# Kernel optimization log

Measured on AMD Instinct MI355X. Metric: run time of the kernel, lower is better.

## Reference

```python
import jax, jax.numpy as jnp
import numpy as np

N = 50000
D = 64
E = 800000


def setup_inputs() -> dict:
    key = jax.random.key(0)
    ks = jax.random.split(key, 8)
    x = jax.random.normal(ks[0], (N, D), dtype=jnp.float32)
    edge_index = jax.random.randint(ks[1], (2, E), 0, N, dtype=jnp.int64)
    edge_attr = jax.random.normal(ks[2], (E,), dtype=jnp.float32)
    x_agg_emb = jax.random.normal(ks[3], (N, D), dtype=jnp.float32)
    # Linear(2D -> D) weights stored as [in, out]; scale ~ kaiming-ish
    W_msg = jax.random.normal(ks[4], (2 * D, D), dtype=jnp.float32) * (1.0 / np.sqrt(2 * D))
    b_msg = jnp.zeros((D,), dtype=jnp.float32)
    W_upd = jax.random.normal(ks[5], (2 * D, D), dtype=jnp.float32) * (1.0 / np.sqrt(2 * D))
    b_upd = jnp.zeros((D,), dtype=jnp.float32)
    return {"x": x, "edge_index": edge_index, "edge_attr": edge_attr,
            "x_agg_emb": x_agg_emb, "W_msg": W_msg, "b_msg": b_msg,
            "W_upd": W_upd, "b_upd": b_upd}


def reference(x, edge_index, edge_attr, x_agg_emb, W_msg, b_msg, W_upd, b_upd):
    col, row = edge_index[0], edge_index[1]
    # edge-weighted gather: [E, D]
    msgs = edge_attr[:, None] * x[col]
    # scatter-mean over destination nodes (dim_size = N)
    summed = jax.ops.segment_sum(msgs, row, num_segments=N)            # [N, D]
    counts = jax.ops.segment_sum(jnp.ones_like(edge_attr), row, num_segments=N)  # [N]
    x_agg = summed / jnp.maximum(counts, 1.0)[:, None]
    # message MLP: Linear(2D->D) + ReLU
    m = jax.nn.relu(jnp.concatenate([x_agg, x_agg_emb], axis=-1) @ W_msg + b_msg)
    # update MLP: Linear(2D->D) + ReLU
    out = jax.nn.relu(jnp.concatenate([x, m], axis=-1) @ W_upd + b_upd)
    return out
```

## Files before the change

kernel.cpp:

```cpp
#include <hip/hip_runtime.h>


#define CAP 48
#define FILLB 2048

typedef __attribute__((ext_vector_type(8))) short short8;
typedef __attribute__((ext_vector_type(4))) float f32x4;

__device__ __forceinline__ unsigned short f2bf(float f) {
    unsigned int u = __float_as_uint(f);
    u += 0x7FFFu + ((u >> 16) & 1u);
    return (unsigned short)(u >> 16);
}
__device__ __forceinline__ uint4 pack8(const float* v) {
    uint4 r;
    r.x = (unsigned)f2bf(v[0]) | ((unsigned)f2bf(v[1]) << 16);
    r.y = (unsigned)f2bf(v[2]) | ((unsigned)f2bf(v[3]) << 16);
    r.z = (unsigned)f2bf(v[4]) | ((unsigned)f2bf(v[5]) << 16);
    r.w = (unsigned)f2bf(v[6]) | ((unsigned)f2bf(v[7]) << 16);
    return r;
}

__global__ __launch_bounds__(256) void zero_f32(float* p, int n) {
    int i = blockIdx.x * 256 + threadIdx.x;
    if (i < n) p[i] = 0.0f;
}
__global__ __launch_bounds__(256) void zero_i32(int* p, int n) {
    int i = blockIdx.x * 256 + threadIdx.x;
    if (i < n) p[i] = 0;
}

__global__ __launch_bounds__(256) void fill_group_kernel(
    const int* __restrict__ ei, const float* __restrict__ ea,
    int* cnt, int2* __restrict__ packed, int E, int N)
{
    const int g   = blockIdx.x & 7;
    const int bg  = blockIdx.x >> 3;
    const int nb  = gridDim.x >> 3;
    const int rpg = (N + 7) >> 3;
    const int rlo = g * rpg;
    const int rhi = min(rlo + rpg, N);
    const int chunk = (E + nb - 1) / nb;
    const int lo = bg * chunk;
    const int hi = min(lo + chunk, E);
    int e = lo + (int)threadIdx.x;
    for (; e + 768 < hi; e += 1024) {
        int r0 = ei[E + e];
        int r1 = ei[E + e + 256];
        int r2 = ei[E + e + 512];
        int r3 = ei[E + e + 768];
        int c0 = ei[e], c1 = ei[e + 256], c2 = ei[e + 512], c3 = ei[e + 768];
        float a0 = ea[e], a1 = ea[e + 256], a2 = ea[e + 512], a3 = ea[e + 768];
        bool m0 = (r0 >= rlo) & (r0 < rhi);
        bool m1 = (r1 >= rlo) & (r1 < rhi);
        bool m2 = (r2 >= rlo) & (r2 < rhi);
        bool m3 = (r3 >= rlo) & (r3 < rhi);
        int p0 = CAP, p1 = CAP, p2 = CAP, p3 = CAP;
        if (m0) p0 = atomicAdd(&cnt[r0], 1);
        if (m1) p1 = atomicAdd(&cnt[r1], 1);
        if (m2) p2 = atomicAdd(&cnt[r2], 1);
        if (m3) p3 = atomicAdd(&cnt[r3], 1);
        if (m0 && p0 < CAP) packed[(size_t)r0 * CAP + p0] = make_int2(c0, __float_as_int(a0));
        if (m1 && p1 < CAP) packed[(size_t)r1 * CAP + p1] = make_int2(c1, __float_as_int(a1));
        if (m2 && p2 < CAP) packed[(size_t)r2 * CAP + p2] = make_int2(c2, __float_as_int(a2));
        if (m3 && p3 < CAP) packed[(size_t)r3 * CAP + p3] = make_int2(c3, __float_as_int(a3));
    }
    for (; e < hi; e += 256) {
        int row = ei[E + e];
        if (row >= rlo && row < rhi) {
            int pos = atomicAdd(&cnt[row], 1);
            if (pos < CAP)
                packed[(size_t)row * CAP + pos] = make_int2(ei[e], __float_as_int(ea[e]));
        }
    }
}


__device__ __forceinline__ void stage_W1024(
    unsigned short* Wb, const float* Wg, int t)
{
    int R = t >> 6, nn = t & 63;
    int kt = R >> 2, qq = R & 3;
    const float* src = Wg + (size_t)(kt * 32 + qq * 8) * 64 + nn;
    float v[8];
    #pragma unroll
    for (int j = 0; j < 8; j++) v[j] = src[(size_t)j * 64];
    *(uint4*)&Wb[R * 528 + nn * 8] = pack8(v);
}

__global__ __launch_bounds__(1024) void gather_mlp(
    const int2* __restrict__ packed, const int* __restrict__ cnt,
    const float* __restrict__ x, const float* __restrict__ emb,
    const float* __restrict__ Wm, const float* __restrict__ bm,
    const float* __restrict__ Wu, const float* __restrict__ bu,
    float* __restrict__ out, int N)
{
    __shared__ __align__(16) unsigned short Ab[64 * 128];
    __shared__ __align__(16) unsigned short Wb[16 * 528];

    const int t    = threadIdx.x;
    const int g    = blockIdx.x & 7;
    const int tile = blockIdx.x >> 3;
    const int rpg  = (N + 7) >> 3;
    const int rlo  = g * rpg;
    const int rhi  = min(rlo + rpg, N);
    const int tile0 = rlo + tile * 64;
    const int w    = t >> 6;
    const int lane = t & 63;
    const int q = lane >> 4, ln = lane & 15;

    stage_W1024(Wb, Wm, t);
    if (t < 512) {
        int r = t >> 3, c = t & 7;
        int node = tile0 + r;
        float v[8] = {0.f, 0.f, 0.f, 0.f, 0.f, 0.f, 0.f, 0.f};
        if (node < rhi) {
            const float* src = emb + (size_t)node * 64 + c * 8;
            float4 p0 = ((const float4*)src)[0];
            float4 p1 = ((const float4*)src)[1];
            v[0] = p0.x; v[1] = p0.y; v[2] = p0.z; v[3] = p0.w;
            v[4] = p1.x; v[5] = p1.y; v[6] = p1.z; v[7] = p1.w;
        }
        int ch = 8 + c;
        *(uint4*)&Ab[r * 128 + ((ch ^ (r & 15)) * 8)] = pack8(v);
    }

    for (int i = 0; i < 4; i++) {
        int r = w * 4 + i;
        int node = tile0 + r;
        float mean = 0.f;
        if (node < rhi) {
            const int2* seg = packed + (size_t)node * CAP;
            int deg = cnt[node];
            int dl = min(deg, CAP);
            float a0 = 0.f, a1 = 0.f, a2 = 0.f, a3 = 0.f;
            int j = 0;
            for (; j + 4 <= dl; j += 4) {
                int4 q0 = ((const int4*)seg)[(j >> 1)];
                int4 q1 = ((const int4*)seg)[(j >> 1) + 1];
                a0 += __int_as_float(q0.y) * x[(size_t)q0.x * 64 + lane];
                a1 += __int_as_float(q0.w) * x[(size_t)q0.z * 64 + lane];
                a2 += __int_as_float(q1.y) * x[(size_t)q1.x * 64 + lane];
                a3 += __int_as_float(q1.w) * x[(size_t)q1.z * 64 + lane];
            }
            for (; j < dl; j++) {
                int2 p = seg[j];
                a0 += __int_as_float(p.y) * x[(size_t)p.x * 64 + lane];
            }
            mean = ((a0 + a1) + (a2 + a3)) / fmaxf((float)deg, 1.0f);
        }
        int ch = lane >> 3;
        Ab[r * 128 + ((ch ^ (r & 15)) * 8) + (lane & 7)] = f2bf(mean);
    }
    __syncthreads();

    const int wr = w & 3, wn = w >> 2;
    f32x4 acc = (f32x4){0.f, 0.f, 0.f, 0.f};
    {
        const int rr = wr * 16 + ln;
        #pragma unroll
        for (int kt = 0; kt < 4; kt++) {
            short8 af = *(const short8*)&Ab[rr * 128 + (((kt * 4 + q) ^ ln) * 8)];
            short8 bf = *(const short8*)&Wb[(kt * 4 + q) * 528 + (wn * 16 + ln) * 8];
            acc = __builtin_amdgcn_mfma_f32_16x16x32_bf16(af, bf, acc, 0, 0, 0);
        }
    }
    __syncthreads();

    stage_W1024(Wb, Wu, t);
    if (t < 512) {
        int r = t >> 3, c = t & 7;
        int node = tile0 + r;
        float v[8] = {0.f, 0.f, 0.f, 0.f, 0.f, 0.f, 0.f, 0.f};
        if (node < rhi) {
            const float* src = x + (size_t)node * 64 + c * 8;
            float4 p0 = ((const float4*)src)[0];
            float4 p1 = ((const float4*)src)[1];
            v[0] = p0.x; v[1] = p0.y; v[2] = p0.z; v[3] = p0.w;
            v[4] = p1.x; v[5] = p1.y; v[6] = p1.z; v[7] = p1.w;
        }
        *(uint4*)&Ab[r * 128 + ((c ^ (r & 15)) * 8)] = pack8(v);
    }
    {
        float bmv = bm[wn * 16 + ln];
        #pragma unroll
        for (int reg = 0; reg < 4; reg++) {
            float mv = fmaxf(acc[reg] + bmv, 0.f);
            int rr = wr * 16 + q * 4 + reg;
            int k  = 64 + wn * 16 + ln;
            int ch = k >> 3;
            Ab[rr * 128 + ((ch ^ (rr & 15)) * 8) + (k & 7)] = f2bf(mv);
        }
    }
    __syncthreads();

    f32x4 acc2 = (f32x4){0.f, 0.f, 0.f, 0.f};
    {
        const int rr = wr * 16 + ln;
        #pragma unroll
        for (int kt = 0; kt < 4; kt++) {
            short8 af = *(const short8*)&Ab[rr * 128 + (((kt * 4 + q) ^ ln) * 8)];
            short8 bf = *(const short8*)&Wb[(kt * 4 + q) * 528 + (wn * 16 + ln) * 8];
            acc2 = __builtin_amdgcn_mfma_f32_16x16x32_bf16(af, bf, acc2, 0, 0, 0);
        }
    }
    {
        float buv = bu[wn * 16 + ln];
        #pragma unroll
        for (int reg = 0; reg < 4; reg++) {
            int rr = wr * 16 + q * 4 + reg;
            int node = tile0 + rr;
            if (node < rhi)
                out[(size_t)node * 64 + wn * 16 + ln] =
                    fmaxf(acc2[reg] + buv, 0.f);
        }
    }
}


__global__ __launch_bounds__(256) void hist_kernel(
    const int* __restrict__ ei, int* hist, int E)
{
    int e = blockIdx.x * 256 + threadIdx.x;
    if (e < E) atomicAdd(&hist[ei[E + e]], 1);
}
__global__ __launch_bounds__(256) void scan_partial_kernel(
    const int* __restrict__ hist, int* partial, int N)
{
    __shared__ int s[256];
    int t = threadIdx.x;
    int i = blockIdx.x * 256 + t;
    s[t] = (i < N) ? hist[i] : 0;
    __syncthreads();
    #pragma unroll
    for (int off = 128; off > 0; off >>= 1) {
        if (t < off) s[t] += s[t + off];
        __syncthreads();
    }
    if (t == 0) partial[blockIdx.x] = s[0];
}
__global__ __launch_bounds__(256) void scan_top_kernel(
    const int* __restrict__ partial, int* scanP, int NB)
{
    __shared__ int s[256];
    int t = threadIdx.x;
    int v = (t < NB) ? partial[t] : 0;
    s[t] = v;
    __syncthreads();
    #pragma unroll
    for (int off = 1; off < 256; off <<= 1) {
        int add = (t >= off) ? s[t - off] : 0;
        __syncthreads();
        s[t] += add;
        __syncthreads();
    }
    if (t < NB) scanP[t] = s[t] - v;
}
__global__ __launch_bounds__(256) void scan_final_kernel(
    const int* __restrict__ hist, const int* __restrict__ scanP,
    int* offsets, int* cursor, int N)
{
    __shared__ int s[256];
    int t = threadIdx.x;
    int i = blockIdx.x * 256 + t;
    int v = (i < N) ? hist[i] : 0;
    s[t] = v;
    __syncthreads();
    #pragma unroll
    for (int off = 1; off < 256; off <<= 1) {
        int add = (t >= off) ? s[t - off] : 0;
        __syncthreads();
        s[t] += add;
        __syncthreads();
    }
    if (i < N) {
        int o = scanP[blockIdx.x] + s[t] - v;
        offsets[i] = o;
        cursor[i]  = o;
    }
}
__global__ __launch_bounds__(256) void fill_kernel(
    const int* __restrict__ ei, const float* __restrict__ ea,
    int* cursor, int2* __restrict__ packed, int E)
{
    int e = blockIdx.x * 256 + threadIdx.x;
    if (e >= E) return;
    int pos = atomicAdd(&cursor[ei[E + e]], 1);
    packed[pos] = make_int2(ei[e], __float_as_int(ea[e]));
}
__global__ __launch_bounds__(256) void gather_kernel(
    const int2* __restrict__ packed, const int* __restrict__ offsets,
    const int* __restrict__ hist, const float* __restrict__ x,
    float* __restrict__ out, int N)
{
    int t = threadIdx.x;
    int n = blockIdx.x * 4 + (t >> 6);
    int lane = t & 63;
    if (n >= N) return;
    int start = offsets[n];
    int deg   = hist[n];
    float a0 = 0.f, a1 = 0.f, a2 = 0.f, a3 = 0.f;
    int j = 0;
    for (; j + 4 <= deg; j += 4) {
        int2 p0 = packed[start + j];
        int2 p1 = packed[start + j + 1];
        int2 p2 = packed[start + j + 2];
        int2 p3 = packed[start + j + 3];
        a0 += __int_as_float(p0.y) * x[(size_t)p0.x * 64 + lane];
        a1 += __int_as_float(p1.y) * x[(size_t)p1.x * 64 + lane];
        a2 += __int_as_float(p2.y) * x[(size_t)p2.x * 64 + lane];
        a3 += __int_as_float(p3.y) * x[(size_t)p3.x * 64 + lane];
    }
    for (; j < deg; j++) {
        int2 p = packed[start + j];
        a0 += __int_as_float(p.y) * x[(size_t)p.x * 64 + lane];
    }
    float acc = (a0 + a1) + (a2 + a3);
    out[(size_t)n * 64 + lane] = acc / fmaxf((float)deg, 1.0f);
}


__global__ __launch_bounds__(256) void scatter_kernel(
    const int* __restrict__ ei, const float* __restrict__ ea,
    const float* __restrict__ x, float* summed, float* counts, int E)
{
    int idx = blockIdx.x * 256 + threadIdx.x;
    int e = idx >> 6;
    int d = idx & 63;
    if (e >= E) return;
    float v = ea[e] * x[(size_t)ei[e] * 64 + d];
    atomicAdd(&summed[(size_t)ei[E + e] * 64 + d], v);
    if (d == 0) atomicAdd(&counts[ei[E + e]], 1.0f);
}


__device__ __forceinline__ void stage_W(
    unsigned short* Wb, const float* Wg, int t)
{
    #pragma unroll
    for (int c = t; c < 1024; c += 256) {
        int R = c >> 6, nn = c & 63;
        int kt = R >> 2, qq = R & 3;
        const float* src = Wg + (size_t)(kt * 32 + qq * 8) * 64 + nn;
        float v[8];
        #pragma unroll
        for (int j = 0; j < 8; j++) v[j] = src[(size_t)j * 64];
        *(uint4*)&Wb[R * 528 + nn * 8] = pack8(v);
    }
}

__device__ __forceinline__ void mfma_tile(
    const unsigned short* Ab, const unsigned short* Wb,
    int wv, int lane, f32x4 acc[4])
{
    const int q  = lane >> 4;
    const int ln = lane & 15;
    const int rr = wv * 16 + ln;
    short8 af[4];
    #pragma unroll
    for (int kt = 0; kt < 4; kt++)
        af[kt] = *(const short8*)&Ab[rr * 128 + (((kt * 4 + q) ^ ln) * 8)];
    #pragma unroll
    for (int nt = 0; nt < 4; nt++) {
        #pragma unroll
        for (int kt = 0; kt < 4; kt++) {
            short8 bf = *(const short8*)&Wb[(kt * 4 + q) * 528 + (nt * 16 + ln) * 8];
            acc[nt] = __builtin_amdgcn_mfma_f32_16x16x32_bf16(af[kt], bf, acc[nt], 0, 0, 0);
        }
    }
}

__global__ __launch_bounds__(256) void mfma_mlp(
    const float* Aagg, const float* __restrict__ Aemb,
    const float* __restrict__ counts, const float* __restrict__ Xin,
    const float* __restrict__ Wm, const float* __restrict__ bm,
    const float* __restrict__ Wu, const float* __restrict__ bu,
    float* out, int N)
{
    __shared__ __align__(16) unsigned short Ab[64 * 128];
    __shared__ __align__(16) unsigned short Wb[16 * 528];

    const int t = threadIdx.x;
    const int tile0 = blockIdx.x * 64;
    const int lane = t & 63, wv = t >> 6;
    const int q = lane >> 4, ln = lane & 15;

    stage_W(Wb, Wm, t);
    #pragma unroll
    for (int s = t; s < 1024; s += 256) {
        int r = s >> 4, chunk = s & 15;
        int node = tile0 + r;
        float v[8] = {0.f, 0.f, 0.f, 0.f, 0.f, 0.f, 0.f, 0.f};
        if (node < N) {
            const float* src = (chunk < 8)
                ? (Aagg + (size_t)node * 64 + chunk * 8)
                : (Aemb + (size_t)node * 64 + (chunk - 8) * 8);
            float4 p0 = ((const float4*)src)[0];
            float4 p1 = ((const float4*)src)[1];
            v[0] = p0.x; v[1] = p0.y; v[2] = p0.z; v[3] = p0.w;
            v[4] = p1.x; v[5] = p1.y; v[6] = p1.z; v[7] = p1.w;
            if (counts && chunk < 8) {
                float rc = 1.0f / fmaxf(counts[node], 1.0f);
                #pragma unroll
                for (int i = 0; i < 8; i++) v[i] *= rc;
            }
        }
        *(uint4*)&Ab[r * 128 + ((chunk ^ (r & 15)) * 8)] = pack8(v);
    }
    __syncthreads();

    f32x4 acc[4];
    #pragma unroll
    for (int nt = 0; nt < 4; nt++) acc[nt] = (f32x4){0.f, 0.f, 0.f, 0.f};
    mfma_tile(Ab, Wb, wv, lane, acc);
    __syncthreads();

    stage_W(Wb, Wu, t);
    #pragma unroll
    for (int s = t; s < 512; s += 256) {
        int r = s >> 3, chunk = s & 7;
        int node = tile0 + r;
        float v[8] = {0.f, 0.f, 0.f, 0.f, 0.f, 0.f, 0.f, 0.f};
        if (node < N) {
            const float* src = Xin + (size_t)node * 64 + chunk * 8;
            float4 p0 = ((const float4*)src)[0];
            float4 p1 = ((const float4*)src)[1];
            v[0] = p0.x; v[1] = p0.y; v[2] = p0.z; v[3] = p0.w;
            v[4] = p1.x; v[5] = p1.y; v[6] = p1.z; v[7] = p1.w;
        }
        *(uint4*)&Ab[r * 128 + ((chunk ^ (r & 15)) * 8)] = pack8(v);
    }
    #pragma unroll
    for (int nt = 0; nt < 4; nt++) {
        float bmv = bm[nt * 16 + ln];
        #pragma unroll
        for (int reg = 0; reg < 4; reg++) {
            float mv = fmaxf(acc[nt][reg] + bmv, 0.f);
            int rr = wv * 16 + q * 4 + reg;
            int k  = 64 + nt * 16 + ln;
            int ch = k >> 3;
            Ab[rr * 128 + ((ch ^ (rr & 15)) * 8) + (k & 7)] = f2bf(mv);
        }
    }
    __syncthreads();

    f32x4 acc2[4];
    #pragma unroll
    for (int nt = 0; nt < 4; nt++) acc2[nt] = (f32x4){0.f, 0.f, 0.f, 0.f};
    mfma_tile(Ab, Wb, wv, lane, acc2);
    #pragma unroll
    for (int nt = 0; nt < 4; nt++) {
        float buv = bu[nt * 16 + ln];
        #pragma unroll
        for (int reg = 0; reg < 4; reg++) {
            int rr = wv * 16 + q * 4 + reg;
            int node = tile0 + rr;
            if (node < N)
                out[(size_t)node * 64 + nt * 16 + ln] =
                    fmaxf(acc2[nt][reg] + buv, 0.f);
        }
    }
}

extern "C" void kernel_launch(void* const* d_in, const int* in_sizes, int n_in,
                              void* d_out, int out_size, void* d_ws, size_t ws_size,
                              hipStream_t stream) {
    const float* x   = (const float*)d_in[0];
    const int*   ei  = (const int*)d_in[1];
    const float* ea  = (const float*)d_in[2];
    const float* emb = (const float*)d_in[3];
    const float* Wm  = (const float*)d_in[4];
    const float* bm  = (const float*)d_in[5];
    const float* Wu  = (const float*)d_in[6];
    const float* bu  = (const float*)d_in[7];
    float*       out = (float*)d_out;

    const int N = in_sizes[0] / 64;
    const int E = in_sizes[2];
    const int NB = (N + 255) / 256;

    const int eblocks = (E + 255) / 256;
    const int mblocks = (N + 63) / 64;
    const int rpg = (N + 7) / 8;

    const size_t need_cap = (size_t)N * CAP * 8 + (size_t)N * 4;
    const size_t need_csr = (size_t)E * 8 + ((size_t)3 * N + 512) * 4;

    if (ws_size >= need_cap) {
        char* ws = (char*)d_ws;
        int2* packed = (int2*)ws;
        int*  cnt    = (int*)(ws + (size_t)N * CAP * 8);

        zero_i32<<<NB, 256, 0, stream>>>(cnt, N);
        fill_group_kernel<<<FILLB, 256, 0, stream>>>(ei, ea, cnt, packed, E, N);
        int tpg = (rpg + 63) / 64;
        gather_mlp<<<8 * tpg, 1024, 0, stream>>>(packed, cnt, x, emb,
                                                 Wm, bm, Wu, bu, out, N);
    } else if (ws_size >= need_csr && NB <= 256) {
        char* ws = (char*)d_ws;
        int2* packed  = (int2*)ws;
        int*  hist    = (int*)(ws + (size_t)E * 8);
        int*  offsets = hist + N;
        int*  cursor  = offsets + N;
        int*  partial = cursor + N;
        int*  scanP   = partial + 256;

        zero_i32<<<NB, 256, 0, stream>>>(hist, N);
        hist_kernel<<<eblocks, 256, 0, stream>>>(ei, hist, E);
        scan_partial_kernel<<<NB, 256, 0, stream>>>(hist, partial, N);
        scan_top_kernel<<<1, 256, 0, stream>>>(partial, scanP, NB);
        scan_final_kernel<<<NB, 256, 0, stream>>>(hist, scanP, offsets, cursor, N);
        fill_kernel<<<eblocks, 256, 0, stream>>>(ei, ea, cursor, packed, E);
        gather_kernel<<<(N + 3) / 4, 256, 0, stream>>>(packed, offsets, hist, x, out, N);
        mfma_mlp<<<mblocks, 256, 0, stream>>>(out, emb, nullptr, x,
                                              Wm, bm, Wu, bu, out, N);
    } else {
        float* counts = (float*)d_ws;
        zero_f32<<<(N * 64 + 255) / 256, 256, 0, stream>>>(out, N * 64);
        zero_f32<<<NB, 256, 0, stream>>>(counts, N);
        long long total = (long long)E * 64;
        scatter_kernel<<<(int)((total + 255) / 256), 256, 0, stream>>>(
            ei, ea, x, out, counts, E);
        mfma_mlp<<<mblocks, 256, 0, stream>>>(out, emb, counts, x,
                                              Wm, bm, Wu, bu, out, N);
    }
}
```

Measured before the change: 175.0 us.

## Gather bf16 copy of x, double-buffer LDS to drop a barrier

Adds a pre-pass that converts x to bf16 into workspace and also zeroes the degree counters, replacing the separate zero kernel. The gather then reads half-width rows, and its inner loop is unrolled to 8 independent accumulators. Both weight matrices and the x tile are staged into separate LDS buffers up front, which removes a barrier and the mid-kernel restaging between the two MLP stages. This trades an extra conversion kernel, more workspace and doubled LDS use (which may reduce occupancy) for less gather bandwidth, and the gathered x values now lose precision to bf16.

Result: faster. 167.2 us (-4.5%).

```diff
diff --git a/kernel.cpp b/kernel.cpp
--- a/kernel.cpp
+++ b/kernel.cpp
@@ -11,6 +11,9 @@
     unsigned int u = __float_as_uint(f);
     u += 0x7FFFu + ((u >> 16) & 1u);
     return (unsigned short)(u >> 16);
+}
+__device__ __forceinline__ float bf2f(unsigned short h) {
+    return __uint_as_float((unsigned)h << 16);
 }
 __device__ __forceinline__ uint4 pack8(const float* v) {
     uint4 r;
@@ -28,6 +31,23 @@
 __global__ __launch_bounds__(256) void zero_i32(int* p, int n) {
     int i = blockIdx.x * 256 + threadIdx.x;
     if (i < n) p[i] = 0;
+}
+
+__global__ __launch_bounds__(256) void cvt_zero(
+    const float* __restrict__ x, unsigned short* __restrict__ xh,
+    int* __restrict__ cnt, int N)
+{
+    int id = blockIdx.x * 256 + threadIdx.x;
+    if (id < N * 8) {
+        const float* src = x + (size_t)id * 8;
+        float4 p0 = ((const float4*)src)[0];
+        float4 p1 = ((const float4*)src)[1];
+        float v[8];
+        v[0] = p0.x; v[1] = p0.y; v[2] = p0.z; v[3] = p0.w;
+        v[4] = p1.x; v[5] = p1.y; v[6] = p1.z; v[7] = p1.w;
+        *(uint4*)&xh[(size_t)id * 8] = pack8(v);
+    }
+    if (id < N) cnt[id] = 0;
 }
 
 __global__ __launch_bounds__(256) void fill_group_kernel(
@@ -90,13 +110,15 @@
 
 __global__ __launch_bounds__(1024) void gather_mlp(
     const int2* __restrict__ packed, const int* __restrict__ cnt,
-    const float* __restrict__ x, const float* __restrict__ emb,
+    const unsigned short* __restrict__ xh, const float* __restrict__ emb,
     const float* __restrict__ Wm, const float* __restrict__ bm,
     const float* __restrict__ Wu, const float* __restrict__ bu,
     float* __restrict__ out, int N)
 {
-    __shared__ __align__(16) unsigned short Ab[64 * 128];
-    __shared__ __align__(16) unsigned short Wb[16 * 528];
+    __shared__ __align__(16) unsigned short Ab [64 * 128];
+    __shared__ __align__(16) unsigned short Ab2[64 * 128];
+    __shared__ __align__(16) unsigned short Wb [16 * 528];
+    __shared__ __align__(16) unsigned short Wb2[16 * 528];
 
     const int t    = threadIdx.x;
     const int g    = blockIdx.x & 7;
@@ -109,9 +131,18 @@
     const int lane = t & 63;
     const int q = lane >> 4, ln = lane & 15;
 
-    stage_W1024(Wb, Wm, t);
+    stage_W1024(Wb,  Wm, t);
+    stage_W1024(Wb2, Wu, t);
     if (t < 512) {
         int r = t >> 3, c = t & 7;
+        int node = tile0 + r;
+        uint4 d = make_uint4(0u, 0u, 0u, 0u);
+        if (node < rhi)
+            d = *(const uint4*)&xh[(size_t)node * 64 + c * 8];
+        *(uint4*)&Ab2[r * 128 + ((c ^ (r & 15)) * 8)] = d;
+    } else {
+        int s = t - 512;
+        int r = s >> 3, c = s & 7;
         int node = tile0 + r;
         float v[8] = {0.f, 0.f, 0.f, 0.f, 0.f, 0.f, 0.f, 0.f};
         if (node < rhi) {
@@ -125,30 +156,51 @@
         *(uint4*)&Ab[r * 128 + ((ch ^ (r & 15)) * 8)] = pack8(v);
     }
 
+    int degs[4];
+    #pragma unroll
+    for (int i = 0; i < 4; i++) {
+        int node = tile0 + w * 4 + i;
+        degs[i] = (node < rhi) ? cnt[node] : 0;
+    }
+    #pragma unroll
     for (int i = 0; i < 4; i++) {
         int r = w * 4 + i;
         int node = tile0 + r;
-        float mean = 0.f;
-        if (node < rhi) {
-            const int2* seg = packed + (size_t)node * CAP;
-            int deg = cnt[node];
-            int dl = min(deg, CAP);
-            float a0 = 0.f, a1 = 0.f, a2 = 0.f, a3 = 0.f;
-            int j = 0;
-            for (; j + 4 <= dl; j += 4) {
-                int4 q0 = ((const int4*)seg)[(j >> 1)];
-                int4 q1 = ((const int4*)seg)[(j >> 1) + 1];
-                a0 += __int_as_float(q0.y) * x[(size_t)q0.x * 64 + lane];
-                a1 += __int_as_float(q0.w) * x[(size_t)q0.z * 64 + lane];
-                a2 += __int_as_float(q1.y) * x[(size_t)q1.x * 64 + lane];
-                a3 += __int_as_float(q1.w) * x[(size_t)q1.z * 64 + lane];
-            }
-            for (; j < dl; j++) {
-                int2 p = seg[j];
-                a0 += __int_as_float(p.y) * x[(size_t)p.x * 64 + lane];
-            }
-            mean = ((a0 + a1) + (a2 + a3)) / fmaxf((float)deg, 1.0f);
-        }
+        int deg = degs[i];
+        int dl = min(deg, CAP);
+        const int2* seg = packed + (size_t)node * CAP;
+        float a0 = 0.f, a1 = 0.f, a2 = 0.f, a3 = 0.f;
+        float a4 = 0.f, a5 = 0.f, a6 = 0.f, a7 = 0.f;
+        int j = 0;
+        for (; j + 8 <= dl; j += 8) {
+            int4 q0 = ((const int4*)seg)[(j >> 1)];
+            int4 q1 = ((const int4*)seg)[(j >> 1) + 1];
+            int4 q2 = ((const int4*)seg)[(j >> 1) + 2];
+            int4 q3 = ((const int4*)seg)[(j >> 1) + 3];
+            a0 += __int_as_float(q0.y) * bf2f(xh[(q0.x << 6) | lane]);
+            a1 += __int_as_float(q0.w) * bf2f(xh[(q0.z << 6) | lane]);
+            a2 += __int_as_float(q1.y) * bf2f(xh[(q1.x << 6) | lane]);
+            a3 += __int_as_float(q1.w) * bf2f(xh[(q1.z << 6) | lane]);
+            a4 += __int_as_float(q2.y) * bf2f(xh[(q2.x << 6) | lane]);
+            a5 += __int_as_float(q2.w) * bf2f(xh[(q2.z << 6) | lane]);
+            a6 += __int_as_float(q3.y) * bf2f(xh[(q3.x << 6) | lane]);
+            a7 += __int_as_float(q3.w) * bf2f(xh[(q3.z << 6) | lane]);
+        }
+        for (; j + 4 <= dl; j += 4) {
+            int4 q0 = ((const int4*)seg)[(j >> 1)];
+            int4 q1 = ((const int4*)seg)[(j >> 1) + 1];
+            a0 += __int_as_float(q0.y) * bf2f(xh[(q0.x << 6) | lane]);
+            a1 += __int_as_float(q0.w) * bf2f(xh[(q0.z << 6) | lane]);
+            a2 += __int_as_float(q1.y) * bf2f(xh[(q1.x << 6) | lane]);
+            a3 += __int_as_float(q1.w) * bf2f(xh[(q1.z << 6) | lane]);
+        }
+        for (; j < dl; j++) {
+            int2 p = seg[j];
+            a0 += __int_as_float(p.y) * bf2f(xh[(p.x << 6) | lane]);
+        }
+        float mean = (((a0 + a1) + (a2 + a3)) + ((a4 + a5) + (a6 + a7)))
+                     / fmaxf((float)deg, 1.0f);
+        if (node >= rhi) mean = 0.f;
         int ch = lane >> 3;
         Ab[r * 128 + ((ch ^ (r & 15)) * 8) + (lane & 7)] = f2bf(mean);
     }
@@ -165,22 +217,7 @@
             acc = __builtin_amdgcn_mfma_f32_16x16x32_bf16(af, bf, acc, 0, 0, 0);
         }
     }
-    __syncthreads();
-
-    stage_W1024(Wb, Wu, t);
-    if (t < 512) {
-        int r = t >> 3, c = t & 7;
-        int node = tile0 + r;
-        float v[8] = {0.f, 0.f, 0.f, 0.f, 0.f, 0.f, 0.f, 0.f};
-        if (node < rhi) {
-            const float* src = x + (size_t)node * 64 + c * 8;
-            float4 p0 = ((const float4*)src)[0];
-            float4 p1 = ((const float4*)src)[1];
-            v[0] = p0.x; v[1] = p0.y; v[2] = p0.z; v[3] = p0.w;
-            v[4] = p1.x; v[5] = p1.y; v[6] = p1.z; v[7] = p1.w;
-        }
-        *(uint4*)&Ab[r * 128 + ((c ^ (r & 15)) * 8)] = pack8(v);
-    }
+
     {
         float bmv = bm[wn * 16 + ln];
         #pragma unroll
@@ -189,7 +226,7 @@
             int rr = wr * 16 + q * 4 + reg;
             int k  = 64 + wn * 16 + ln;
             int ch = k >> 3;
-            Ab[rr * 128 + ((ch ^ (rr & 15)) * 8) + (k & 7)] = f2bf(mv);
+            Ab2[rr * 128 + ((ch ^ (rr & 15)) * 8) + (k & 7)] = f2bf(mv);
         }
     }
     __syncthreads();
@@ -199,8 +236,8 @@
         const int rr = wr * 16 + ln;
         #pragma unroll
         for (int kt = 0; kt < 4; kt++) {
-            short8 af = *(const short8*)&Ab[rr * 128 + (((kt * 4 + q) ^ ln) * 8)];
-            short8 bf = *(const short8*)&Wb[(kt * 4 + q) * 528 + (wn * 16 + ln) * 8];
+            short8 af = *(const short8*)&Ab2[rr * 128 + (((kt * 4 + q) ^ ln) * 8)];
+            short8 bf = *(const short8*)&Wb2[(kt * 4 + q) * 528 + (wn * 16 + ln) * 8];
             acc2 = __builtin_amdgcn_mfma_f32_16x16x32_bf16(af, bf, acc2, 0, 0, 0);
         }
     }
@@ -483,18 +520,20 @@
     const int mblocks = (N + 63) / 64;
     const int rpg = (N + 7) / 8;
 
-    const size_t need_cap = (size_t)N * CAP * 8 + (size_t)N * 4;
+    const size_t need_cap = (size_t)N * CAP * 8 + (size_t)N * 128 + (size_t)N * 4;
     const size_t need_csr = (size_t)E * 8 + ((size_t)3 * N + 512) * 4;
 
     if (ws_size >= need_cap) {
         char* ws = (char*)d_ws;
-        int2* packed = (int2*)ws;
-        int*  cnt    = (int*)(ws + (size_t)N * CAP * 8);
-
-        zero_i32<<<NB, 256, 0, stream>>>(cnt, N);
+        int2*           packed = (int2*)ws;
+        unsigned short* xh     = (unsigned short*)(ws + (size_t)N * CAP * 8);
+        int*            cnt    = (int*)(ws + (size_t)N * CAP * 8 + (size_t)N * 128);
+
+        int cb = (N * 8 + 255) / 256;
+        cvt_zero<<<cb, 256, 0, stream>>>(x, xh, cnt, N);
         fill_group_kernel<<<FILLB, 256, 0, stream>>>(ei, ea, cnt, packed, E, N);
         int tpg = (rpg + 63) / 64;
-        gather_mlp<<<8 * tpg, 1024, 0, stream>>>(packed, cnt, x, emb,
+        gather_mlp<<<8 * tpg, 1024, 0, stream>>>(packed, cnt, xh, emb,
                                                  Wm, bm, Wu, bu, out, N);
     } else if (ws_size >= need_csr && NB <= 256) {
         char* ws = (char*)d_ws;
```
